# Kernel optimization log

Measured on AMD Instinct MI355X. Metric: run time of the kernel, lower is better.

## Reference

```python
import jax, jax.numpy as jnp
import numpy as np

B, S = 32, 256          # batch, sequence
D = 128                 # d_model
I = 256                 # mamba intermediate = 2*D
N = 16                  # ssm state size
R = 8                   # dt rank = ceil(D/16)
K = 4                   # conv kernel
L = 4                   # num mamba layers
Z = 128                 # vib z_dim
FUT = 20                # future steps


def setup_inputs() -> dict:
    key = jax.random.key(0)
    ks = iter(jax.random.split(key, 40))

    def nrm(shape, scale=0.02):
        return jax.random.normal(next(ks), shape, dtype=jnp.float32) * scale

    return {
        "x_cam": jax.random.normal(next(ks), (B, S, 8, 1024), dtype=jnp.float32),
        "x_ego": jax.random.normal(next(ks), (B, S, 64), dtype=jnp.float32),
        "vib_eps": jax.random.normal(next(ks), (B, Z), dtype=jnp.float32),
        "vis_w1": nrm((8 * 1024, 512)), "vis_b1": jnp.zeros((512,), jnp.float32),
        "vis_w2": nrm((512, D)), "vis_b2": jnp.zeros((D,), jnp.float32),
        "ego_w": nrm((64, D)), "ego_b": jnp.zeros((D,), jnp.float32),
        "fus_w": nrm((2 * D, D)), "fus_b": jnp.zeros((D,), jnp.float32),
        "norm_w": jnp.ones((L, D), jnp.float32),
        "in_proj_w": nrm((L, D, 2 * I)),
        "conv_w": nrm((L, I, K), 0.1), "conv_b": jnp.zeros((L, I), jnp.float32),
        "x_proj_w": nrm((L, I, R + 2 * N)),
        "dt_proj_w": nrm((L, R, I), 0.1), "dt_proj_b": jnp.full((L, I), -2.0, jnp.float32),
        "A_log": jnp.tile(jnp.log(jnp.arange(1, N + 1, dtype=jnp.float32))[None, None, :], (L, I, 1)),
        "D_par": jnp.ones((L, I), jnp.float32),
        "out_proj_w": nrm((L, I, D)),
        "normf_w": jnp.ones((D,), jnp.float32),
        "mu_w": nrm((D, Z)), "mu_b": jnp.zeros((Z,), jnp.float32),
        "lv_w": nrm((D, Z)), "lv_b": jnp.zeros((Z,), jnp.float32),
        "h1_w": nrm((Z, 256)), "h1_b": jnp.zeros((256,), jnp.float32),
        "h2_w": nrm((256, FUT * 2)), "h2_b": jnp.zeros((FUT * 2,), jnp.float32),
    }


def _rms(x, w, eps=1e-5):
    return x * jax.lax.rsqrt(jnp.mean(x * x, axis=-1, keepdims=True) + eps) * w


def _mixer(x, inw, cw, cb, xpw, dtw, dtb, alog, dpar, outw):
    # x: [B,S,D]
    Bb, Ss, _ = x.shape
    h, gate = jnp.split(x @ inw, 2, axis=-1)            # [B,S,I] each
    # depthwise causal conv (kernel K)
    hp = jnp.pad(h, ((0, 0), (K - 1, 0), (0, 0)))
    h = sum(hp[:, k:k + Ss, :] * cw[:, k] for k in range(K)) + cb
    h = jax.nn.silu(h)
    ssm = h @ xpw                                        # [B,S,R+2N]
    dt = jax.nn.softplus(ssm[..., :R] @ dtw + dtb)       # [B,S,I]
    Bm = ssm[..., R:R + N]                               # [B,S,N]
    Cm = ssm[..., R + N:]                                # [B,S,N]
    A = -jnp.exp(alog)                                   # [I,N]
    dA = jnp.exp(dt[..., None] * A)                      # [B,S,I,N]
    dBu = dt[..., None] * Bm[:, :, None, :] * h[..., None]  # [B,S,I,N]

    def step(carry, t):
        dA_t, dBu_t, C_t = t
        carry = carry * dA_t + dBu_t                     # [B,I,N]
        return carry, jnp.einsum('bin,bn->bi', carry, C_t)

    h0 = jnp.zeros((Bb, I, N), dtype=x.dtype)
    _, ys = jax.lax.scan(step, h0, (dA.swapaxes(0, 1), dBu.swapaxes(0, 1), Cm.swapaxes(0, 1)))
    y = ys.swapaxes(0, 1) + h * dpar                     # [B,S,I]
    y = y * jax.nn.silu(gate)
    return y @ outw                                      # [B,S,D]


def _mamba(x, norm_w, in_proj_w, conv_w, conv_b, x_proj_w, dt_proj_w, dt_proj_b, A_log, D_par, out_proj_w, normf_w):
    for l in range(L):
        x = x + _mixer(_rms(x, norm_w[l]), in_proj_w[l], conv_w[l], conv_b[l],
                       x_proj_w[l], dt_proj_w[l], dt_proj_b[l], A_log[l], D_par[l], out_proj_w[l])
    return _rms(x, normf_w)


def _forward(x_cam, x_ego, vib_eps, vis_w1, vis_b1, vis_w2, vis_b2, ego_w, ego_b, fus_w, fus_b,
             norm_w, in_proj_w, conv_w, conv_b, x_proj_w, dt_proj_w, dt_proj_b, A_log, D_par,
             out_proj_w, normf_w, mu_w, mu_b, lv_w, lv_b, h1_w, h1_b, h2_w, h2_b):
    Bb, Ss = x_cam.shape[:2]
    v = x_cam.reshape(Bb, Ss, -1)                                          # [B,S,8192]
    v = jax.nn.gelu(v @ vis_w1 + vis_b1, approximate=False) @ vis_w2 + vis_b2
    e = x_ego @ ego_w + ego_b
    fused = jax.nn.gelu(jnp.concatenate([v, e], axis=-1) @ fus_w + fus_b, approximate=False)
    h = _mamba(fused, norm_w, in_proj_w, conv_w, conv_b, x_proj_w,
               dt_proj_w, dt_proj_b, A_log, D_par, out_proj_w, normf_w)
    last = h[:, -1, :]                                                     # [B,D]
    mu = last @ mu_w + mu_b
    logvar = last @ lv_w + lv_b
    z = mu + vib_eps * jnp.exp(0.5 * logvar)
    kl = -0.5 * jnp.mean(1.0 + logvar - mu * mu - jnp.exp(logvar))
    out = jax.nn.relu(z @ h1_w + h1_b) @ h2_w + h2_b
    return out.reshape(Bb, FUT, 2), kl


def reference(x_cam, x_ego, vib_eps, vis_w1, vis_b1, vis_w2, vis_b2, ego_w, ego_b, fus_w, fus_b,
              norm_w, in_proj_w, conv_w, conv_b, x_proj_w, dt_proj_w, dt_proj_b, A_log, D_par,
              out_proj_w, normf_w, mu_w, mu_b, lv_w, lv_b, h1_w, h1_b, h2_w, h2_b):
    return _forward(x_cam, x_ego, vib_eps, vis_w1, vis_b1, vis_w2, vis_b2, ego_w, ego_b, fus_w, fus_b,
                    norm_w, in_proj_w, conv_w, conv_b, x_proj_w, dt_proj_w, dt_proj_b, A_log, D_par,
                    out_proj_w, normf_w, mu_w, mu_b, lv_w, lv_b, h1_w, h1_b, h2_w, h2_b)
```

## Files before the change

kernel.cpp:

```cpp
#include <hip/hip_runtime.h>
#include <hip/hip_bf16.h>
#include <math.h>

#define BQ 32
#define SQ 256
#define MTOK 8192
#define DD 128
#define II 256
#define NNs 16
#define RRs 8
#define KKs 4
#define LLs 4
#define ZZs 128
#define FUTs 20

typedef __attribute__((ext_vector_type(8))) short bf8v;
typedef __attribute__((ext_vector_type(4))) float f4v;

__device__ __forceinline__ float geluf(float x){ return 0.5f*x*(1.0f+erff(x*0.70710678118654752f)); }
__device__ __forceinline__ float siluf(float x){ return x/(1.0f+__expf(-x)); }
__device__ __forceinline__ float softplusf(float x){ return fmaxf(x,0.0f)+log1pf(__expf(-fabsf(x))); }
__device__ __forceinline__ unsigned short f2bf(float x){
    __hip_bfloat16 h = __float2bfloat16(x);
    return *reinterpret_cast<unsigned short*>(&h);
}

__device__ __forceinline__ void gload_lds16(const void* g, void* l){
    __builtin_amdgcn_global_load_lds(
        (const __attribute__((address_space(1))) void*)g,
        (__attribute__((address_space(3))) void*)l, 16, 0, 0);
}

template<int ACT,int ADD,int OUTBF>
__launch_bounds__(256,2)
__global__ void gemm_lds_kernel(const unsigned short* __restrict__ A,
                                const unsigned short* __restrict__ Bt,
                                const float* __restrict__ bias,
                                void* __restrict__ Cv,
                                int M, int N, int Kd, int ldc)
{
    __shared__ unsigned short As[2][128*64];
    __shared__ unsigned short Bs[2][64*64];
    const int tid = threadIdx.x;
    const int w = tid >> 6, lane = tid & 63;
    const int ml = lane & 15, quad = lane >> 4;
    const int rowBase = blockIdx.x * 128, colBase = blockIdx.y * 64;

    const int srow = w*8 + (lane>>3);
    const int scol = (((lane&7) ^ (lane>>3)))*8;

    f4v acc[2][4];
    #pragma unroll
    for (int i=0;i<2;i++)
      #pragma unroll
      for (int j=0;j<4;j++) acc[i][j] = (f4v){0.f,0.f,0.f,0.f};

    auto stage = [&](int buf, int kt){
        #pragma unroll
        for (int e=0;e<4;e++){
            const unsigned short* src = A + (size_t)(rowBase + srow + e*32)*Kd + kt + scol;
            gload_lds16(src, (unsigned short*)As[buf] + (w + e*4)*512);
        }
        #pragma unroll
        for (int e=0;e<2;e++){
            const unsigned short* src = Bt + (size_t)(colBase + srow + e*32)*Kd + kt + scol;
            gload_lds16(src, (unsigned short*)Bs[buf] + (w + e*4)*512);
        }
    };

    stage(0, 0);
    __syncthreads();

    const int swz = (ml&7)*8;
    int cur = 0;
    for (int kt=0; kt<Kd; kt+=64){
        if (kt + 64 < Kd) stage(cur^1, kt+64);
        #pragma unroll
        for (int ks=0; ks<2; ks++){
            const int co = (ks*32 + quad*8) ^ swz;
            bf8v a0 = *reinterpret_cast<const bf8v*>(&As[cur][(w*32 +      ml)*64 + co]);
            bf8v a1 = *reinterpret_cast<const bf8v*>(&As[cur][(w*32 + 16 + ml)*64 + co]);
            #pragma unroll
            for (int nt=0; nt<4; nt++){
                bf8v b = *reinterpret_cast<const bf8v*>(&Bs[cur][(nt*16+ml)*64 + co]);
                acc[0][nt] = __builtin_amdgcn_mfma_f32_16x16x32_bf16(a0, b, acc[0][nt], 0,0,0);
                acc[1][nt] = __builtin_amdgcn_mfma_f32_16x16x32_bf16(a1, b, acc[1][nt], 0,0,0);
            }
        }
        __syncthreads();
        cur ^= 1;
    }

    #pragma unroll
    for (int mt=0; mt<2; mt++){
        #pragma unroll
        for (int nt=0; nt<4; nt++){
            int col = colBase + nt*16 + ml;
            float bb = bias ? bias[col] : 0.0f;
            #pragma unroll
            for (int r=0;r<4;r++){
                int row = rowBase + w*32 + mt*16 + quad*4 + r;
                float v = acc[mt][nt][r] + bb;
                if (ACT==1) v = geluf(v);
                if constexpr (OUTBF==1){
                    ((unsigned short*)Cv)[(size_t)row*ldc + col] = f2bf(v);
                } else {
                    float* cp = (float*)Cv + (size_t)row*ldc + col;
                    if (ADD) v += *cp;
                    *cp = v;
                }
            }
        }
    }
}

template<int ACT,int ADD,int OUTBF,typename AT>
__launch_bounds__(256,2)
__global__ void gemm_bf16_kernel(const AT* __restrict__ A,
                                 const unsigned short* __restrict__ Bt,
                                 const float* __restrict__ bias,
                                 void* __restrict__ Cv,
                                 int M, int N, int Kd, int ldc)
{
    constexpr int LDK = 72;
    __shared__ unsigned short As[128*LDK];
    __shared__ unsigned short Bs[64*LDK];
    const int tid = threadIdx.x;
    const int w = tid >> 6, lane = tid & 63;
    const int ml = lane & 15, quad = lane >> 4;
    const int rowBase = blockIdx.x * 128, colBase = blockIdx.y * 64;

    f4v acc[2][4];
    #pragma unroll
    for (int i=0;i<2;i++)
      #pragma unroll
      for (int j=0;j<4;j++) acc[i][j] = (f4v){0.f,0.f,0.f,0.f};

    bf8v pa[4], pb[2];
    const int ar = tid >> 3, as8 = (tid & 7) * 8;

    auto loadTile = [&](int kt){
        #pragma unroll
        for (int e=0;e<4;e++){
            int r = ar + e*32;
            if constexpr (sizeof(AT)==2){
                pa[e] = *reinterpret_cast<const bf8v*>(
                    (const unsigned short*)A + (size_t)(rowBase+r)*Kd + kt + as8);
            } else {
                const float* ap = (const float*)A + (size_t)(rowBase+r)*Kd + kt + as8;
                float4 v0 = *reinterpret_cast<const float4*>(ap);
                float4 v1 = *reinterpret_cast<const float4*>(ap+4);
                union { unsigned short u[8]; bf8v v; } o;
                o.u[0]=f2bf(v0.x); o.u[1]=f2bf(v0.y); o.u[2]=f2bf(v0.z); o.u[3]=f2bf(v0.w);
                o.u[4]=f2bf(v1.x); o.u[5]=f2bf(v1.y); o.u[6]=f2bf(v1.z); o.u[7]=f2bf(v1.w);
                pa[e] = o.v;
            }
        }
        #pragma unroll
        for (int e=0;e<2;e++){
            int r = ar + e*32;
            pb[e] = *reinterpret_cast<const bf8v*>(
                Bt + (size_t)(colBase+r)*Kd + kt + as8);
        }
    };

    loadTile(0);

    for (int kt=0; kt<Kd; kt+=64){
        #pragma unroll
        for (int e=0;e<4;e++) *reinterpret_cast<bf8v*>(&As[(ar+e*32)*LDK + as8]) = pa[e];
        #pragma unroll
        for (int e=0;e<2;e++) *reinterpret_cast<bf8v*>(&Bs[(ar+e*32)*LDK + as8]) = pb[e];
        __syncthreads();
        if (kt + 64 < Kd) loadTile(kt + 64);
        #pragma unroll
        for (int ks=0; ks<2; ks++){
            bf8v a0 = *reinterpret_cast<bf8v*>(&As[(w*32 +      ml)*LDK + ks*32 + quad*8]);
            bf8v a1 = *reinterpret_cast<bf8v*>(&As[(w*32 + 16 + ml)*LDK + ks*32 + quad*8]);
            #pragma unroll
            for (int nt=0; nt<4; nt++){
                bf8v b = *reinterpret_cast<bf8v*>(&Bs[(nt*16+ml)*LDK + ks*32 + quad*8]);
                acc[0][nt] = __builtin_amdgcn_mfma_f32_16x16x32_bf16(a0, b, acc[0][nt], 0,0,0);
                acc[1][nt] = __builtin_amdgcn_mfma_f32_16x16x32_bf16(a1, b, acc[1][nt], 0,0,0);
            }
        }
        __syncthreads();
    }

    #pragma unroll
    for (int mt=0; mt<2; mt++){
        #pragma unroll
        for (int nt=0; nt<4; nt++){
            int col = colBase + nt*16 + ml;
            float bb = bias ? bias[col] : 0.0f;
            #pragma unroll
            for (int r=0;r<4;r++){
                int row = rowBase + w*32 + mt*16 + quad*4 + r;
                float v = acc[mt][nt][r] + bb;
                if (ACT==1) v = geluf(v);
                if constexpr (OUTBF==1){
                    ((unsigned short*)Cv)[(size_t)row*ldc + col] = f2bf(v);
                } else {
                    float* cp = (float*)Cv + (size_t)row*ldc + col;
                    if (ADD) v += *cp;
                    *cp = v;
                }
            }
        }
    }
}

__launch_bounds__(256)
__global__ void cast_bf16_kernel(const float* __restrict__ in, unsigned short* __restrict__ out)
{
    size_t i = (size_t)blockIdx.x*256 + threadIdx.x;
    const float4 v0 = reinterpret_cast<const float4*>(in)[i*2];
    const float4 v1 = reinterpret_cast<const float4*>(in)[i*2+1];
    union { unsigned short u[8]; bf8v v; } o;
    o.u[0]=f2bf(v0.x); o.u[1]=f2bf(v0.y); o.u[2]=f2bf(v0.z); o.u[3]=f2bf(v0.w);
    o.u[4]=f2bf(v1.x); o.u[5]=f2bf(v1.y); o.u[6]=f2bf(v1.z); o.u[7]=f2bf(v1.w);
    reinterpret_cast<bf8v*>(out)[i] = o.v;
}

__launch_bounds__(256)
__global__ void castT_kernel(const float* __restrict__ in, unsigned short* __restrict__ out,
                             int Kd, int N)
{
    __shared__ float t[64][65];
    int k0 = blockIdx.y*64, n0 = blockIdx.x*64;
    int c = threadIdx.x & 63, r4 = threadIdx.x >> 6;
    #pragma unroll
    for (int it=0; it<16; it++){
        int row = it*4 + r4;
        t[row][c] = in[(size_t)(k0+row)*N + n0 + c];
    }
    __syncthreads();
    #pragma unroll
    for (int it=0; it<16; it++){
        int row = it*4 + r4;
        out[(size_t)(n0+row)*Kd + k0 + c] = f2bf(t[c][row]);
    }
}

__launch_bounds__(256)
__global__ void rms_bf_kernel(const float* __restrict__ x, const float* __restrict__ w,
                              unsigned short* __restrict__ out)
{
    int tid = threadIdx.x;
    int lane = tid & 63, wv = tid >> 6;
    int token = blockIdx.x*4 + wv;
    const float* xr = x + (size_t)token*DD;
    float v0 = xr[lane], v1 = xr[lane+64];
    float ss = v0*v0 + v1*v1;
    #pragma unroll
    for (int off=32; off>0; off>>=1) ss += __shfl_xor(ss, off);
    float r = rsqrtf(ss*(1.0f/DD) + 1e-5f);
    unsigned short* o = out + (size_t)token*DD;
    o[lane]    = f2bf(v0*r*w[lane]);
    o[lane+64] = f2bf(v1*r*w[lane+64]);
}

__launch_bounds__(256)
__global__ void conv_kernel(const float* __restrict__ hg, const float* __restrict__ cw,
                            const float* __restrict__ cb, float* __restrict__ hc)
{
    int idx = blockIdx.x*256 + threadIdx.x;
    int i = idx & (II-1);
    int m = idx >> 8;
    int s = m & (SQ-1);
    const float* w = cw + i*KKs;
    float a = cb[i];
    #pragma unroll
    for (int k=0;k<KKs;k++){
        int ssrc = s + k - (KKs-1);
        if (ssrc >= 0) a += hg[(size_t)(m + k - (KKs-1))*(2*II) + i] * w[k];
    }
    hc[idx] = siluf(a);
}

#define XT 16
__launch_bounds__(256)
__global__ void xproj_fused_kernel(const float* __restrict__ hconv,
                                   const float* __restrict__ xpw,
                                   const float* __restrict__ dtw,
                                   const float* __restrict__ dtb,
                                   float* __restrict__ dt_out,
                                   float* __restrict__ bc)
{
    __shared__ float sh[XT][II+4];
    __shared__ float ssm_s[XT][40];
    const int tid = threadIdx.x;
    const int m0 = blockIdx.x * XT;

    {
        const float4* src = reinterpret_cast<const float4*>(hconv + (size_t)m0*II);
        #pragma unroll
        for (int e=0;e<4;e++){
            int idx = e*256 + tid;
            int t = idx >> 6, c = idx & 63;
            *reinterpret_cast<float4*>(&sh[t][c*4]) = src[idx];
        }
    }
    __syncthreads();

    for (int e = tid; e < XT*40; e += 256){
        int t = e / 40, o = e - t*40;
        float a0=0.f, a1=0.f, a2=0.f, a3=0.f;
        #pragma unroll 16
        for (int k=0;k<II;k+=4){
            float4 h4 = *reinterpret_cast<const float4*>(&sh[t][k]);
            a0 += h4.x*xpw[(k+0)*40+o];
            a1 += h4.y*xpw[(k+1)*40+o];
            a2 += h4.z*xpw[(k+2)*40+o];
            a3 += h4.w*xpw[(k+3)*40+o];
        }
        ssm_s[t][o] = (a0+a1)+(a2+a3);
    }
    __syncthreads();

    #pragma unroll
    for (int e = tid; e < XT*32; e += 256){
        int t = e >> 5, n = e & 31;
        bc[(size_t)(m0+t)*32 + n] = ssm_s[t][8+n];
    }

    {
        const int i = tid;
        float wr[RRs];
        #pragma unroll
        for (int r=0;r<RRs;r++) wr[r] = dtw[r*II + i];
        const float bb = dtb[i];
        #pragma unroll 4
        for (int t=0;t<XT;t++){
            float a = bb;
            #pragma unroll
            for (int r=0;r<RRs;r++) a += ssm_s[t][r]*wr[r];
            dt_out[(size_t)(m0+t)*II + i] = softplusf(a);
        }
    }
}

__launch_bounds__(256)
__global__ void scan_kernel(const float* __restrict__ dtp, const float* __restrict__ bc,
                            const float* __restrict__ hconv, const float* __restrict__ hg,
                            const float* __restrict__ A_log, const float* __restrict__ D_par,
                            unsigned short* __restrict__ ybf)
{
    __shared__ float sdt[16][17], shv[16][17], sgv[16][17], sbc[16][33];
    int b = blockIdx.x >> 4, chunk = blockIdx.x & 15;
    int tid = threadIdx.x;
    int n = tid & 15, il = tid >> 4;
    int i = chunk*16 + il;
    float A2 = -__expf(A_log[i*NNs + n]) * 1.44269504f;
    float carry = 0.0f;
    const float dpi = D_par[i];
    const int m0 = b*SQ;
    const int li = tid & 15, ls = tid >> 4;
    const int gi = chunk*16 + li;
    for (int cs=0; cs<16; cs++){
        __syncthreads();
        int mload = m0 + cs*16 + ls;
        sdt[ls][li] = dtp[(size_t)mload*II + gi];
        shv[ls][li] = hconv[(size_t)mload*II + gi];
        sgv[ls][li] = hg[(size_t)mload*(2*II) + II + gi];
        sbc[ls][li]      = bc[(size_t)mload*32 + li];
        sbc[ls][li + 16] = bc[(size_t)mload*32 + 16 + li];
        __syncthreads();
        #pragma unroll
        for (int s=0; s<16; s++){
            float dtv = sdt[s][il];
            float hv  = shv[s][il];
            float dA  = exp2f(dtv*A2);
            carry = carry*dA + dtv*hv*sbc[s][n];
            float acc = carry*sbc[s][16+n];
            acc += __shfl_xor(acc, 1);
            acc += __shfl_xor(acc, 2);
            acc += __shfl_xor(acc, 4);
            acc += __shfl_xor(acc, 8);
            if (n == 0){
                ybf[(size_t)(m0 + cs*16 + s)*II + i] =
                    f2bf((acc + hv*dpi) * siluf(sgv[s][il]));
            }
        }
    }
}

__launch_bounds__(128)
__global__ void head_kernel(const float* __restrict__ x, const float* __restrict__ normf,
                            const float* __restrict__ mu_w, const float* __restrict__ mu_b,
                            const float* __restrict__ lv_w, const float* __restrict__ lv_b,
                            const float* __restrict__ eps, const float* __restrict__ h1_w,
                            const float* __restrict__ h1_b, const float* __restrict__ h2_w,
                            const float* __restrict__ h2_b, float* __restrict__ out,
                            float* __restrict__ klacc)
{
    __shared__ float lasts[DD];
    __shared__ float zs[DD];
    __shared__ float hr[256];
    __shared__ float red[2];
    int b = blockIdx.x, d = threadIdx.x;
    int lane = d & 63, wv = d >> 6;
    float xv = x[((size_t)(b*SQ + SQ-1))*DD + d];
    float ss = xv*xv;
    #pragma unroll
    for (int off=32; off>0; off>>=1) ss += __shfl_xor(ss, off);
    if (lane==0) red[wv] = ss;
    __syncthreads();
    float tot = red[0] + red[1];
    float last = xv * rsqrtf(tot*(1.0f/DD) + 1e-5f) * normf[d];
    lasts[d] = last;
    __syncthreads();
    float mu = mu_b[d], lv = lv_b[d];
    for (int j=0;j<DD;j++){
        float lj = lasts[j];
        mu += lj*mu_w[j*DD + d];
        lv += lj*lv_w[j*DD + d];
    }
    float z = mu + eps[b*ZZs + d]*__expf(0.5f*lv);
    zs[d] = z;
    float klp = 1.0f + lv - mu*mu - __expf(lv);
    #pragma unroll
    for (int off=32; off>0; off>>=1) klp += __shfl_xor(klp, off);
    if (lane==0) red[wv] = klp;
    __syncthreads();
    if (d==0) atomicAdd(klacc, red[0]+red[1]);
    for (int o=d; o<256; o+=128){
        float a = h1_b[o];
        for (int j=0;j<DD;j++) a += zs[j]*h1_w[j*256 + o];
        hr[o] = fmaxf(a, 0.0f);
    }
    __syncthreads();
    if (d < 40){
        float a = h2_b[d];
        for (int k=0;k<256;k++) a += hr[k]*h2_w[k*40 + d];
        out[b*(FUTs*2) + d] = a;
    }
}

__global__ void kl_final_kernel(const float* __restrict__ klacc, float* __restrict__ out)
{
    out[0] = -0.5f * klacc[0] * (1.0f/(BQ*ZZs));
}

extern "C" void kernel_launch(void* const* d_in, const int* in_sizes, int n_in,
                              void* d_out, int out_size, void* d_ws, size_t ws_size,
                              hipStream_t stream)
{
    const float* x_cam     = (const float*)d_in[0];
    const float* x_ego     = (const float*)d_in[1];
    const float* vib_eps   = (const float*)d_in[2];
    const float* vis_w1    = (const float*)d_in[3];
    const float* vis_b1    = (const float*)d_in[4];
    const float* vis_w2    = (const float*)d_in[5];
    const float* vis_b2    = (const float*)d_in[6];
    const float* ego_w     = (const float*)d_in[7];
    const float* ego_b     = (const float*)d_in[8];
    const float* fus_w     = (const float*)d_in[9];
    const float* fus_b     = (const float*)d_in[10];
    const float* norm_w    = (const float*)d_in[11];
    const float* in_proj_w = (const float*)d_in[12];
    const float* conv_w    = (const float*)d_in[13];
    const float* conv_b    = (const float*)d_in[14];
    const float* x_proj_w  = (const float*)d_in[15];
    const float* dt_proj_w = (const float*)d_in[16];
    const float* dt_proj_b = (const float*)d_in[17];
    const float* A_log     = (const float*)d_in[18];
    const float* D_par     = (const float*)d_in[19];
    const float* out_proj_w= (const float*)d_in[20];
    const float* normf_w   = (const float*)d_in[21];
    const float* mu_w      = (const float*)d_in[22];
    const float* mu_b      = (const float*)d_in[23];
    const float* lv_w      = (const float*)d_in[24];
    const float* lv_b      = (const float*)d_in[25];
    const float* h1_w      = (const float*)d_in[26];
    const float* h1_b      = (const float*)d_in[27];
    const float* h2_w      = (const float*)d_in[28];
    const float* h2_b      = (const float*)d_in[29];

    float* ws = (float*)d_ws;
    float* hg    = ws;
    unsigned short* v1g  = (unsigned short*)hg;
    float* hconv = ws + 4194304;
    unsigned short* catbf = (unsigned short*)hconv;
    float* xbuf  = ws + 6291456;
    float* dtws  = ws + 7340032;
    float* bcws  = ws + 9437184;
    unsigned short* ybf  = (unsigned short*)(ws + 9699328);
    unsigned short* xnbf = (unsigned short*)(ws + 10747904);
    unsigned short* w1t  = (unsigned short*)(ws + 11272192);
    unsigned short* w2t  = (unsigned short*)(ws + 13369344);
    unsigned short* egot = (unsigned short*)(ws + 13402112);
    unsigned short* fust = (unsigned short*)(ws + 13406208);
    unsigned short* wipt = (unsigned short*)(ws + 13422592);
    unsigned short* wopt = (unsigned short*)(ws + 13553664);
    float* klacc = ws + 13619200;
    unsigned short* xcbf = (unsigned short*)(ws + 13619208);
    const size_t need_bytes = (size_t)(13619208 + 33554432) * 4;
    const bool big_ws = (ws_size >= need_bytes);

    hipMemsetAsync(klacc, 0, sizeof(float), stream);

    castT_kernel<<<dim3(8, 128), 256, 0, stream>>>(vis_w1, w1t, 8192, 512);
    castT_kernel<<<dim3(2, 8),   256, 0, stream>>>(vis_w2, w2t, 512, 128);
    castT_kernel<<<dim3(2, 1),   256, 0, stream>>>(ego_w,  egot, 64, 128);
    castT_kernel<<<dim3(2, 4),   256, 0, stream>>>(fus_w,  fust, 256, 128);
    for (int l=0; l<LLs; l++){
        castT_kernel<<<dim3(8, 2), 256, 0, stream>>>(
            in_proj_w + (size_t)l*DD*2*II, wipt + (size_t)l*2*II*DD, DD, 2*II);
        castT_kernel<<<dim3(2, 4), 256, 0, stream>>>(
            out_proj_w + (size_t)l*II*DD, wopt + (size_t)l*DD*II, II, DD);
    }

    if (big_ws){
        cast_bf16_kernel<<<32768, 256, 0, stream>>>(x_cam, xcbf);
        gemm_lds_kernel<1,0,1><<<dim3(64, 8), 256, 0, stream>>>(
            xcbf, w1t, vis_b1, v1g, MTOK, 512, 8192, 512);
    } else {
        gemm_bf16_kernel<1,0,1,float><<<dim3(64, 8), 256, 0, stream>>>(
            x_cam, w1t, vis_b1, v1g, MTOK, 512, 8192, 512);
    }
    gemm_lds_kernel<0,0,1><<<dim3(64, 2), 256, 0, stream>>>(
        v1g, w2t, vis_b2, catbf, MTOK, 128, 512, 256);
    gemm_bf16_kernel<0,0,1,float><<<dim3(64, 2), 256, 0, stream>>>(
        x_ego, egot, ego_b, catbf + 128, MTOK, 128, 64, 256);
    gemm_lds_kernel<1,0,0><<<dim3(64, 2), 256, 0, stream>>>(
        catbf, fust, fus_b, xbuf, MTOK, 128, 256, 128);

    for (int l=0; l<LLs; l++){
        rms_bf_kernel<<<MTOK/4, 256, 0, stream>>>(xbuf, norm_w + l*DD, xnbf);
        gemm_lds_kernel<0,0,0><<<dim3(64, 8), 256, 0, stream>>>(
            xnbf, wipt + (size_t)l*2*II*DD, nullptr, hg, MTOK, 2*II, DD, 2*II);
        conv_kernel<<<MTOK*II/256, 256, 0, stream>>>(
            hg, conv_w + (size_t)l*II*KKs, conv_b + (size_t)l*II, hconv);
        xproj_fused_kernel<<<MTOK/XT, 256, 0, stream>>>(
            hconv, x_proj_w + (size_t)l*II*40, dt_proj_w + (size_t)l*RRs*II,
            dt_proj_b + (size_t)l*II, dtws, bcws);
        scan_kernel<<<BQ*16, 256, 0, stream>>>(
            dtws, bcws, hconv, hg, A_log + (size_t)l*II*NNs, D_par + (size_t)l*II, ybf);
        gemm_lds_kernel<0,1,0><<<dim3(64, 2), 256, 0, stream>>>(
            ybf, wopt + (size_t)l*DD*II, nullptr, xbuf, MTOK, DD, II, DD);
    }

    head_kernel<<<BQ, 128, 0, stream>>>(
        xbuf, normf_w, mu_w, mu_b, lv_w, lv_b, vib_eps,
        h1_w, h1_b, h2_w, h2_b, (float*)d_out, klacc);
    kl_final_kernel<<<1, 1, 0, stream>>>(klacc, (float*)d_out + 1280);
}
```

Measured before the change: 1.222 ms.

## Triple-buffer GEMM LDS staging with explicit vmcnt waits and barriers

Replaces the double-buffered LDS pipeline in the bf16 MFMA GEMM with a three-stage ring, issuing global->LDS loads two tiles ahead. Partial s_waitcnt vmcnt counts replace a full __syncthreads, so loads for later tiles can stay in flight while the current tile is computed, hiding more global memory latency. LDS use rises to 72KB per block, which may reduce occupancy below the 2 blocks/SM launch bound. The hand-coded vmcnt counts assume exactly 6 loads per stage and at least two K tiles.

```diff
diff --git a/kernel.cpp b/kernel.cpp
--- a/kernel.cpp
+++ b/kernel.cpp
@@ -31,6 +31,20 @@
         (__attribute__((address_space(3))) void*)l, 16, 0, 0);
 }
 
+#define PIPE_WAIT_BAR(N) do {                                   \
+    __builtin_amdgcn_sched_barrier(0);                          \
+    asm volatile("s_waitcnt vmcnt(" #N ")" ::: "memory");       \
+    __builtin_amdgcn_s_barrier();                               \
+    __builtin_amdgcn_sched_barrier(0);                          \
+} while(0)
+
+#define PIPE_END_BAR() do {                                     \
+    __builtin_amdgcn_sched_barrier(0);                          \
+    asm volatile("s_waitcnt lgkmcnt(0)" ::: "memory");          \
+    __builtin_amdgcn_s_barrier();                               \
+    __builtin_amdgcn_sched_barrier(0);                          \
+} while(0)
+
 template<int ACT,int ADD,int OUTBF>
 __launch_bounds__(256,2)
 __global__ void gemm_lds_kernel(const unsigned short* __restrict__ A,
@@ -39,8 +53,8 @@
                                 void* __restrict__ Cv,
                                 int M, int N, int Kd, int ldc)
 {
-    __shared__ unsigned short As[2][128*64];
-    __shared__ unsigned short Bs[2][64*64];
+    __shared__ __align__(16) unsigned short As[3][128*64];
+    __shared__ __align__(16) unsigned short Bs[3][64*64];
     const int tid = threadIdx.x;
     const int w = tid >> 6, lane = tid & 63;
     const int ml = lane & 15, quad = lane >> 4;
@@ -68,28 +82,40 @@
         }
     };
 
-    stage(0, 0);
-    __syncthreads();
-
     const int swz = (ml&7)*8;
-    int cur = 0;
-    for (int kt=0; kt<Kd; kt+=64){
-        if (kt + 64 < Kd) stage(cur^1, kt+64);
+
+    auto compute = [&](int buf){
         #pragma unroll
         for (int ks=0; ks<2; ks++){
             const int co = (ks*32 + quad*8) ^ swz;
-            bf8v a0 = *reinterpret_cast<const bf8v*>(&As[cur][(w*32 +      ml)*64 + co]);
-            bf8v a1 = *reinterpret_cast<const bf8v*>(&As[cur][(w*32 + 16 + ml)*64 + co]);
+            bf8v a0 = *reinterpret_cast<const bf8v*>(&As[buf][(w*32 +      ml)*64 + co]);
+            bf8v a1 = *reinterpret_cast<const bf8v*>(&As[buf][(w*32 + 16 + ml)*64 + co]);
             #pragma unroll
             for (int nt=0; nt<4; nt++){
-                bf8v b = *reinterpret_cast<const bf8v*>(&Bs[cur][(nt*16+ml)*64 + co]);
+                bf8v b = *reinterpret_cast<const bf8v*>(&Bs[buf][(nt*16+ml)*64 + co]);
                 acc[0][nt] = __builtin_amdgcn_mfma_f32_16x16x32_bf16(a0, b, acc[0][nt], 0,0,0);
                 acc[1][nt] = __builtin_amdgcn_mfma_f32_16x16x32_bf16(a1, b, acc[1][nt], 0,0,0);
             }
         }
-        __syncthreads();
-        cur ^= 1;
-    }
+    };
+
+    const int nIter = Kd >> 6;
+    stage(0, 0);
+    stage(1, 64);
+
+    int i = 0;
+    for (; i + 2 < nIter; ++i){
+        stage((i+2)%3, (i+2)<<6);
+        PIPE_WAIT_BAR(12);
+        compute(i%3);
+        PIPE_END_BAR();
+    }
+    PIPE_WAIT_BAR(6);
+    compute(i%3);
+    PIPE_END_BAR();
+    ++i;
+    PIPE_WAIT_BAR(0);
+    compute(i%3);
 
     #pragma unroll
     for (int mt=0; mt<2; mt++){
```

After: 1.214 ms. No clear change (-0.7%).
